# Performance work log

Measured on AMD Instinct MI355X. Metric: run time of the kernel, lower is better.

## Reference

```python
import jax, jax.numpy as jnp
import numpy as np

VOCAB, D = 32000, 1024
EPS = 1e-5

def setup_inputs() -> dict:
    key = jax.random.key(0)
    k1, k2, k3, k4 = jax.random.split(key, 4)
    patch_embeddings = jax.random.normal(k1, (16, 256, D), dtype=jnp.float32)
    text_prototypes = jax.random.normal(k2, (VOCAB, D), dtype=jnp.float32) * 0.02
    # nn.Linear(d, d): weight [d, d], bias [d]
    lim = 1.0 / np.sqrt(D)
    W = jax.random.uniform(k3, (D, D), minval=-lim, maxval=lim, dtype=jnp.float32)
    b = jax.random.uniform(k4, (D,), minval=-lim, maxval=lim, dtype=jnp.float32)
    gamma = jnp.ones((D,), dtype=jnp.float32)
    beta = jnp.zeros((D,), dtype=jnp.float32)
    return {"patch_embeddings": patch_embeddings, "text_prototypes": text_prototypes,
            "W": W, "b": b, "gamma": gamma, "beta": beta}

def _layer_norm(x, gamma, beta):
    mu = jnp.mean(x, axis=-1, keepdims=True)
    var = jnp.mean(jnp.square(x - mu), axis=-1, keepdims=True)
    return (x - mu) * jax.lax.rsqrt(var + EPS) * gamma + beta

def reference(patch_embeddings, text_prototypes, W, b, gamma, beta):
    # similarities: [B, P, V]
    sims = jnp.einsum('bpd,vd->bpv', patch_embeddings, text_prototypes)
    attn = jax.nn.softmax(sims, axis=-1)
    reprogrammed = jnp.einsum('bpv,vd->bpd', attn, text_prototypes)
    transformed = jnp.einsum('bpd,ed->bpe', reprogrammed, W) + b
    return _layer_norm(patch_embeddings + transformed, gamma, beta)
```

## Files before the change

### kernel.cpp

```cpp
#include <hip/hip_runtime.h>
#include <hip/hip_bf16.h>
#include <cstdint>
#include <cstddef>

#define D_DIM 1024
#define VOCAB 32000
#define ROWS  4096
#define KSPLIT2 5

typedef __attribute__((ext_vector_type(8))) short bf16x8;
typedef __attribute__((ext_vector_type(4))) float f32x4;
typedef __attribute__((ext_vector_type(4))) int   i32x4;
typedef __attribute__((ext_vector_type(8))) int   i32x8;

static __device__ __forceinline__ i32x8 cat8(i32x4 lo, i32x4 hi) {
  return __builtin_shufflevector(lo, hi, 0, 1, 2, 3, 4, 5, 6, 7);
}

static __device__ __forceinline__ unsigned short f2bf(float f) {
  union { float f; unsigned int u; } c; c.f = f;
  unsigned int u = c.u;
  u += 0x7fffu + ((u >> 16) & 1u);
  return (unsigned short)(u >> 16);
}

static __device__ __forceinline__ int pk8(float a, float b) {
  return __builtin_amdgcn_cvt_pk_fp8_f32(a, b, 0, false);
}

static __device__ __forceinline__ void gload_lds16(const void* g, void* s) {
  __builtin_amdgcn_global_load_lds(
      (const __attribute__((address_space(1))) uint32_t*)(g),
      (__attribute__((address_space(3))) uint32_t*)(s), 16, 0, 0);
}

__global__ void k_cvt(const float* __restrict__ src, short* __restrict__ dst, int n4) {
  int i = blockIdx.x * 256 + threadIdx.x;
  if (i < n4) {
    float4 v = *(const float4*)(src + (size_t)i * 4);
    ushort4 u;
    u.x = f2bf(v.x); u.y = f2bf(v.y); u.z = f2bf(v.z); u.w = f2bf(v.w);
    *(ushort4*)(dst + (size_t)i * 4) = u;
  }
}

__global__ void k_cvt_q8(const float* __restrict__ src, uint8_t* __restrict__ dst) {
  int i = blockIdx.x * 256 + threadIdx.x;
  float4 a = *(const float4*)(src + (size_t)i * 8);
  float4 b = *(const float4*)(src + (size_t)i * 8 + 4);
  uint2 o;
  o.x = (pk8(a.x, a.y) & 0xffff) | (pk8(a.z, a.w) << 16);
  o.y = (pk8(b.x, b.y) & 0xffff) | (pk8(b.z, b.w) << 16);
  *(uint2*)(dst + (size_t)i * 8) = o;
}

__global__ void k_prep_K8(const float* __restrict__ src, uint8_t* __restrict__ kb,
                          uint8_t* __restrict__ kt, int R, int C) {
  __shared__ uint8_t tile[64][68];
  int t  = threadIdx.x;
  int r0 = blockIdx.x * 64;
  int c0 = blockIdx.y * 64;
  int lr = t >> 4;
  int lc = (t & 15) * 4;
#pragma unroll
  for (int i = 0; i < 4; ++i) {
    int r = lr + 16 * i;
    float4 v = *(const float4*)(src + (size_t)(r0 + r) * C + c0 + lc);
    unsigned p = (pk8(v.x * 64.f, v.y * 64.f) & 0xffff) | (pk8(v.z * 64.f, v.w * 64.f) << 16);
    *(unsigned*)&tile[r][lc] = p;
    *(unsigned*)(kb + (size_t)(r0 + r) * C + c0 + lc) = p;
  }
  __syncthreads();
#pragma unroll
  for (int i = 0; i < 4; ++i) {
    int c = lr + 16 * i;
    unsigned p = tile[lc + 0][c] | (tile[lc + 1][c] << 8) |
                 (tile[lc + 2][c] << 16) | ((unsigned)tile[lc + 3][c] << 24);
    *(unsigned*)(kt + (size_t)(c0 + c) * R + r0 + lc) = p;
  }
}

#define PS8 144
__global__ __launch_bounds__(256) void k_gemm8(
    const uint8_t* __restrict__ A, int lda,
    const uint8_t* __restrict__ B, int ldb,
    int Kdim, int mode,
    uint8_t* __restrict__ Pout, long ldp, float* __restrict__ den,
    float* __restrict__ Cacc)
{
  __shared__ uint8_t smem[32768];
  uint8_t* As = smem;
  uint8_t* Bs = smem + 16384;

  int tid  = threadIdx.x;
  int wave = tid >> 6;
  int lane = tid & 63;
  int quad = lane >> 4;
  int t16  = lane & 15;
  int wy = wave >> 1, wx = wave & 1;

  long mBase, nBase;
  if (mode == 0) { mBase = (long)blockIdx.x * 128; nBase = (long)blockIdx.y * 128; }
  else           { mBase = (long)blockIdx.y * 128; nBase = (long)blockIdx.x * 128; }
  int k0 = blockIdx.z * Kdim;

  const uint8_t* Ab = A + (size_t)mBase * lda + k0;
  const uint8_t* Bb = B + (size_t)nBase * ldb + k0;
  int lrow = lane >> 3;
  int lcol = ((lane & 7) ^ lrow) * 16;

  f32x4 acc[4][4];
#pragma unroll
  for (int i = 0; i < 4; ++i)
#pragma unroll
    for (int j = 0; j < 4; ++j) acc[i][j] = (f32x4){0.f, 0.f, 0.f, 0.f};

  int sw = t16 & 7;
  int co0 = (((quad << 1) ^ sw) << 4);
  const int SC1 = 0x7F7F7F7F;

  for (int kk = 0; kk < Kdim; kk += 128) {
#pragma unroll
    for (int i = 0; i < 4; ++i) {
      int row = wave * 32 + i * 8;
      gload_lds16(Ab + (size_t)(row + lrow) * lda + kk + lcol, &As[row * 128]);
      gload_lds16(Bb + (size_t)(row + lrow) * ldb + kk + lcol, &Bs[row * 128]);
    }
    __syncthreads();
    i32x8 af[4], bfr[4];
#pragma unroll
    for (int mi = 0; mi < 4; ++mi) {
      const uint8_t* rp = &As[(wy * 64 + mi * 16 + t16) * 128];
      af[mi] = cat8(*(const i32x4*)(rp + co0), *(const i32x4*)(rp + (co0 ^ 16)));
    }
#pragma unroll
    for (int ni = 0; ni < 4; ++ni) {
      const uint8_t* rp = &Bs[(wx * 64 + ni * 16 + t16) * 128];
      bfr[ni] = cat8(*(const i32x4*)(rp + co0), *(const i32x4*)(rp + (co0 ^ 16)));
    }
#pragma unroll
    for (int mi = 0; mi < 4; ++mi)
#pragma unroll
      for (int ni = 0; ni < 4; ++ni)
        acc[mi][ni] = __builtin_amdgcn_mfma_scale_f32_16x16x128_f8f6f4(
            af[mi], bfr[ni], acc[mi][ni], 0, 0, 0, SC1, 0, SC1);
    __syncthreads();
  }

  if (mode == 0) {
    float rsum[4][4];
#pragma unroll
    for (int mi = 0; mi < 4; ++mi)
#pragma unroll
      for (int r = 0; r < 4; ++r) rsum[mi][r] = 0.f;
#pragma unroll
    for (int mi = 0; mi < 4; ++mi) {
      int rloc = wy * 64 + mi * 16 + quad * 4;
#pragma unroll
      for (int ni = 0; ni < 4; ++ni) {
        int cloc = wx * 64 + ni * 16 + t16;
#pragma unroll
        for (int r = 0; r < 4; ++r) {
          float e = __expf(acc[mi][ni][r] * 0.015625f);
          smem[(rloc + r) * PS8 + cloc] = (uint8_t)pk8(e, e);
          rsum[mi][r] += e;
        }
      }
    }
#pragma unroll
    for (int mi = 0; mi < 4; ++mi)
#pragma unroll
      for (int r = 0; r < 4; ++r) {
        float s = rsum[mi][r];
        s += __shfl_xor(s, 1);
        s += __shfl_xor(s, 2);
        s += __shfl_xor(s, 4);
        s += __shfl_xor(s, 8);
        if (t16 == 0)
          atomicAdd(&den[mBase + wy * 64 + mi * 16 + quad * 4 + r], s);
      }
    __syncthreads();
    int rr  = tid >> 3;
    int c16 = (tid & 7) * 16;
#pragma unroll
    for (int i = 0; i < 4; ++i) {
      int row = i * 32 + rr;
      i32x4 v = *(const i32x4*)&smem[row * PS8 + c16];
      __builtin_nontemporal_store(v, (i32x4*)&Pout[(size_t)(mBase + row) * ldp + nBase + c16]);
    }
  } else {
#pragma unroll
    for (int mi = 0; mi < 4; ++mi) {
      long row = mBase + wy * 64 + mi * 16 + quad * 4;
#pragma unroll
      for (int ni = 0; ni < 4; ++ni) {
        long col = nBase + wx * 64 + ni * 16 + t16;
#pragma unroll
        for (int r = 0; r < 4; ++r)
          atomicAdd(&Cacc[(size_t)(row + r) * 1024 + col], acc[mi][ni][r]);
      }
    }
  }
}

__global__ __launch_bounds__(256) void k_gemm_bf(
    const short* __restrict__ A, int lda,
    const short* __restrict__ B, int ldb, int Kdim,
    const float* __restrict__ bias, const float* __restrict__ resid,
    float* __restrict__ Cout)
{
  __shared__ short smem[16384];
  short* As = smem;
  short* Bs = smem + 8192;

  int tid  = threadIdx.x;
  int wave = tid >> 6;
  int lane = tid & 63;
  int quad = lane >> 4;
  int t16  = lane & 15;
  int wy = wave >> 1, wx = wave & 1;

  long mBase = (long)blockIdx.y * 128;
  long nBase = (long)blockIdx.x * 128;

  const short* Ab = A + (size_t)mBase * lda;
  const short* Bb = B + (size_t)nBase * ldb;
  int lrow = lane >> 3;
  int lcol = ((lane & 7) ^ lrow) * 8;

  f32x4 acc[4][4];
#pragma unroll
  for (int i = 0; i < 4; ++i)
#pragma unroll
    for (int j = 0; j < 4; ++j) acc[i][j] = (f32x4){0.f, 0.f, 0.f, 0.f};

  int sw = t16 & 7;

  for (int kk = 0; kk < Kdim; kk += 64) {
#pragma unroll
    for (int i = 0; i < 4; ++i) {
      int row = wave * 32 + i * 8;
      gload_lds16(Ab + (size_t)(row + lrow) * lda + kk + lcol, &As[row * 64]);
      gload_lds16(Bb + (size_t)(row + lrow) * ldb + kk + lcol, &Bs[row * 64]);
    }
    __syncthreads();
#pragma unroll
    for (int kc = 0; kc < 8; kc += 4) {
      bf16x8 af[4], bfr[4];
#pragma unroll
      for (int mi = 0; mi < 4; ++mi)
        af[mi] = *(const bf16x8*)&As[(wy * 64 + mi * 16 + t16) * 64 +
                                     (((kc + quad) ^ sw) << 3)];
#pragma unroll
      for (int ni = 0; ni < 4; ++ni)
        bfr[ni] = *(const bf16x8*)&Bs[(wx * 64 + ni * 16 + t16) * 64 +
                                      (((kc + quad) ^ sw) << 3)];
#pragma unroll
      for (int mi = 0; mi < 4; ++mi)
#pragma unroll
        for (int ni = 0; ni < 4; ++ni)
          acc[mi][ni] = __builtin_amdgcn_mfma_f32_16x16x32_bf16(af[mi], bfr[ni],
                                                                acc[mi][ni], 0, 0, 0);
    }
    __syncthreads();
  }

#pragma unroll
  for (int mi = 0; mi < 4; ++mi) {
    long row = mBase + wy * 64 + mi * 16 + quad * 4;
#pragma unroll
    for (int ni = 0; ni < 4; ++ni) {
      long col = nBase + wx * 64 + ni * 16 + t16;
#pragma unroll
      for (int r = 0; r < 4; ++r) {
        size_t idx = (size_t)(row + r) * 1024 + col;
        Cout[idx] = acc[mi][ni][r] + bias[col] + resid[idx];
      }
    }
  }
}

__global__ void k_div(const float* __restrict__ num, const float* __restrict__ den,
                      short* __restrict__ out) {
  int i = (blockIdx.x * 256 + threadIdx.x) * 4;
  float4 v = *(const float4*)(num + i);
  float inv = 0.015625f / den[i >> 10];
  ushort4 u;
  u.x = f2bf(v.x * inv); u.y = f2bf(v.y * inv);
  u.z = f2bf(v.z * inv); u.w = f2bf(v.w * inv);
  *(ushort4*)(out + i) = u;
}

__global__ __launch_bounds__(256) void k_ln(const float* __restrict__ x,
                                            const float* __restrict__ gamma,
                                            const float* __restrict__ beta,
                                            float* __restrict__ out) {
  __shared__ float s_sum[4], s_sq[4];
  int row = blockIdx.x;
  int tid = threadIdx.x;
  const float* xr = x + (size_t)row * 1024;
  float4 v = *(const float4*)(xr + tid * 4);
  float s = v.x + v.y + v.z + v.w;
  float q = v.x * v.x + v.y * v.y + v.z * v.z + v.w * v.w;
#pragma unroll
  for (int off = 32; off >= 1; off >>= 1) {
    s += __shfl_down(s, off);
    q += __shfl_down(q, off);
  }
  int wv = tid >> 6;
  if ((tid & 63) == 0) { s_sum[wv] = s; s_sq[wv] = q; }
  __syncthreads();
  float tot  = s_sum[0] + s_sum[1] + s_sum[2] + s_sum[3];
  float totq = s_sq[0] + s_sq[1] + s_sq[2] + s_sq[3];
  float mu   = tot * (1.0f / 1024.0f);
  float var  = totq * (1.0f / 1024.0f) - mu * mu;
  float rstd = rsqrtf(var + 1e-5f);
  float4 g = *(const float4*)(gamma + tid * 4);
  float4 b = *(const float4*)(beta + tid * 4);
  float4 o;
  o.x = (v.x - mu) * rstd * g.x + b.x;
  o.y = (v.y - mu) * rstd * g.y + b.y;
  o.z = (v.z - mu) * rstd * g.z + b.z;
  o.w = (v.w - mu) * rstd * g.w + b.w;
  *(float4*)(out + (size_t)row * 1024 + tid * 4) = o;
}

extern "C" void kernel_launch(void* const* d_in, const int* in_sizes, int n_in,
                              void* d_out, int out_size, void* d_ws, size_t ws_size,
                              hipStream_t stream) {
  const float* patch = (const float*)d_in[0];
  const float* proto = (const float*)d_in[1];
  const float* W     = (const float*)d_in[2];
  const float* bvec  = (const float*)d_in[3];
  const float* gamma = (const float*)d_in[4];
  const float* beta  = (const float*)d_in[5];
  float* out = (float*)d_out;

  char* ws = (char*)d_ws;
  size_t off = 0;
  uint8_t* Q8  = (uint8_t*)(ws + off); off += (size_t)ROWS * D_DIM;
  uint8_t* Kb8 = (uint8_t*)(ws + off); off += (size_t)VOCAB * D_DIM;
  uint8_t* KT8 = (uint8_t*)(ws + off); off += (size_t)VOCAB * D_DIM;
  short*   Wb  = (short*)(ws + off);   off += (size_t)D_DIM * D_DIM * 2;
  short*   Rb  = (short*)(ws + off);   off += (size_t)ROWS * D_DIM * 2;
  uint8_t* P8  = (uint8_t*)(ws + off); off += (size_t)ROWS * VOCAB;
  float*   num = (float*)(ws + off);   off += (size_t)ROWS * D_DIM * 4;
  float*   den = (float*)(ws + off);   off += (size_t)ROWS * 4;
  float*   pre = (float*)P8;

  hipMemsetAsync(den, 0, ROWS * sizeof(float), stream);
  hipMemsetAsync(num, 0, (size_t)ROWS * D_DIM * sizeof(float), stream);

  k_cvt_q8<<<ROWS * D_DIM / 8 / 256, 256, 0, stream>>>(patch, Q8);
  k_cvt<<<D_DIM * D_DIM / 4 / 256, 256, 0, stream>>>(W, Wb, D_DIM * D_DIM / 4);
  k_prep_K8<<<dim3(VOCAB / 64, D_DIM / 64), 256, 0, stream>>>(proto, Kb8, KT8, VOCAB, D_DIM);

  k_gemm8<<<dim3(ROWS / 128, VOCAB / 128, 1), 256, 0, stream>>>(
      Q8, D_DIM, Kb8, D_DIM, D_DIM, 0,
      P8, (long)VOCAB, den, nullptr);

  k_gemm8<<<dim3(D_DIM / 128, ROWS / 128, KSPLIT2), 256, 0, stream>>>(
      P8, VOCAB, KT8, VOCAB, VOCAB / KSPLIT2, 1,
      nullptr, 0, nullptr, num);

  k_div<<<ROWS * D_DIM / 4 / 256, 256, 0, stream>>>(num, den, Rb);

  k_gemm_bf<<<dim3(D_DIM / 128, ROWS / 128), 256, 0, stream>>>(
      Rb, D_DIM, Wb, D_DIM, D_DIM, bvec, patch, pre);

  k_ln<<<ROWS, 256, 0, stream>>>(pre, gamma, beta, out);
}
```

Before: 684.3 us.

## Replace split-K atomic second GEMM with dedicated 128x256 fp8 kernel writing two partials

The P·K^T GEMM, which used the generic fp8 kernel with a 5-way K split and float atomicAdd into a zeroed buffer, is replaced by a dedicated 512-thread kernel. It uses 128x256 tiles, a 2-way K split, double-buffered async global-to-LDS loads with explicit vmcnt waits, and plain nontemporal stores into two separate partial buffers. k_div now sums the two partials, which removes the memset of the numerator and the atomic traffic. The costs are 96KB of LDS per block, a grid of only 256 blocks, and reuse of the Kb8 workspace as a partial buffer, which depends on Kb8 no longer being needed after the first GEMM.

```diff
diff --git a/kernel.cpp b/kernel.cpp
--- a/kernel.cpp
+++ b/kernel.cpp
@@ -6,7 +6,6 @@
 #define D_DIM 1024
 #define VOCAB 32000
 #define ROWS  4096
-#define KSPLIT2 5
 
 typedef __attribute__((ext_vector_type(8))) short bf16x8;
 typedef __attribute__((ext_vector_type(4))) float f32x4;
@@ -203,6 +202,109 @@
   }
 }
 
+#define G2NT 125
+__global__ __launch_bounds__(512, 2) void k_g2(
+    const uint8_t* __restrict__ P, const uint8_t* __restrict__ KT,
+    float* __restrict__ n0, float* __restrict__ n1)
+{
+  __shared__ uint8_t smem[98304];
+
+  int tid  = threadIdx.x;
+  int wave = tid >> 6;
+  int lane = tid & 63;
+  int quad = lane >> 4;
+  int t16  = lane & 15;
+  int wm = wave >> 2;
+  int wn = wave & 3;
+
+  int xn = blockIdx.x & 3;
+  int zz = (blockIdx.x >> 2) & 1;
+  int ym = blockIdx.x >> 3;
+  long mBase = (long)ym * 128;
+  long nBase = (long)xn * 256;
+  int  k0    = zz * 16000;
+
+  const uint8_t* Ab = P  + (size_t)mBase * VOCAB + k0;
+  const uint8_t* Bb = KT + (size_t)nBase * VOCAB + k0;
+  int lrow = lane >> 3;
+  int lcol = ((lane & 7) ^ lrow) * 16;
+
+  f32x4 acc[4][4];
+#pragma unroll
+  for (int i = 0; i < 4; ++i)
+#pragma unroll
+    for (int j = 0; j < 4; ++j) acc[i][j] = (f32x4){0.f, 0.f, 0.f, 0.f};
+
+  int sw  = t16 & 7;
+  int co0 = (((quad << 1) ^ sw) << 4);
+  const int SC1 = 0x7F7F7F7F;
+
+  auto STAGE = [&](int slot, int t) {
+    uint8_t* As = &smem[slot * 49152];
+    uint8_t* Bs = As + 16384;
+    long kk = (long)t * 128;
+#pragma unroll
+    for (int g = 0; g < 2; ++g) {
+      int r0 = wave * 16 + g * 8;
+      gload_lds16(Ab + (size_t)(r0 + lrow) * VOCAB + kk + lcol, As + r0 * 128);
+    }
+#pragma unroll
+    for (int g = 0; g < 4; ++g) {
+      int r0 = wave * 32 + g * 8;
+      gload_lds16(Bb + (size_t)(r0 + lrow) * VOCAB + kk + lcol, Bs + r0 * 128);
+    }
+  };
+
+  STAGE(0, 0);
+  STAGE(1, 1);
+
+  for (int t = 0; t < G2NT; ++t) {
+    const uint8_t* As = &smem[(t & 1) * 49152];
+    const uint8_t* Bs = As + 16384;
+
+    if (t + 1 < G2NT)
+      asm volatile("s_waitcnt vmcnt(6)\n\ts_barrier" ::: "memory");
+    else
+      asm volatile("s_waitcnt vmcnt(0)\n\ts_barrier" ::: "memory");
+
+    i32x8 af[4], bfr[4];
+#pragma unroll
+    for (int mi = 0; mi < 4; ++mi) {
+      const uint8_t* rp = As + (wm * 64 + mi * 16 + t16) * 128;
+      af[mi] = cat8(*(const i32x4*)(rp + co0), *(const i32x4*)(rp + (co0 ^ 16)));
+    }
+#pragma unroll
+    for (int ni = 0; ni < 4; ++ni) {
+      const uint8_t* rp = Bs + (wn * 64 + ni * 16 + t16) * 128;
+      bfr[ni] = cat8(*(const i32x4*)(rp + co0), *(const i32x4*)(rp + (co0 ^ 16)));
+    }
+    __builtin_amdgcn_s_setprio(1);
+#pragma unroll
+    for (int mi = 0; mi < 4; ++mi)
+#pragma unroll
+      for (int ni = 0; ni < 4; ++ni)
+        acc[mi][ni] = __builtin_amdgcn_mfma_scale_f32_16x16x128_f8f6f4(
+            af[mi], bfr[ni], acc[mi][ni], 0, 0, 0, SC1, 0, SC1);
+    __builtin_amdgcn_s_setprio(0);
+    asm volatile("s_barrier" ::: "memory");
+    if (t + 2 < G2NT) STAGE(t & 1, t + 2);
+  }
+
+  float* outp = zz ? n1 : n0;
+#pragma unroll
+  for (int mi = 0; mi < 4; ++mi) {
+    long row = mBase + wm * 64 + mi * 16 + quad * 4;
+#pragma unroll
+    for (int ni = 0; ni < 4; ++ni) {
+      long col = nBase + wn * 64 + ni * 16 + t16;
+#pragma unroll
+      for (int r = 0; r < 4; ++r)
+        __builtin_nontemporal_store(acc[mi][ni][r],
+                                    &outp[(size_t)(row + r) * D_DIM + col]);
+    }
+  }
+}
+
 __global__ __launch_bounds__(256) void k_gemm_bf(
     const short* __restrict__ A, int lda,
     const short* __restrict__ B, int ldb, int Kdim,
@@ -280,14 +382,15 @@
   }
 }
 
-__global__ void k_div(const float* __restrict__ num, const float* __restrict__ den,
-                      short* __restrict__ out) {
+__global__ void k_div(const float* __restrict__ n0, const float* __restrict__ n1,
+                      const float* __restrict__ den, short* __restrict__ out) {
   int i = (blockIdx.x * 256 + threadIdx.x) * 4;
-  float4 v = *(const float4*)(num + i);
+  float4 a = *(const float4*)(n0 + i);
+  float4 b = *(const float4*)(n1 + i);
   float inv = 0.015625f / den[i >> 10];
   ushort4 u;
-  u.x = f2bf(v.x * inv); u.y = f2bf(v.y * inv);
-  u.z = f2bf(v.z * inv); u.w = f2bf(v.w * inv);
+  u.x = f2bf((a.x + b.x) * inv); u.y = f2bf((a.y + b.y) * inv);
+  u.z = f2bf((a.z + b.z) * inv); u.w = f2bf((a.w + b.w) * inv);
   *(ushort4*)(out + i) = u;
 }
 
@@ -347,9 +450,10 @@
   float*   num = (float*)(ws + off);   off += (size_t)ROWS * D_DIM * 4;
   float*   den = (float*)(ws + off);   off += (size_t)ROWS * 4;
   float*   pre = (float*)P8;
+  float*   nz0 = (float*)Kb8;
+  float*   nz1 = num;
 
   hipMemsetAsync(den, 0, ROWS * sizeof(float), stream);
-  hipMemsetAsync(num, 0, (size_t)ROWS * D_DIM * sizeof(float), stream);
 
   k_cvt_q8<<<ROWS * D_DIM / 8 / 256, 256, 0, stream>>>(patch, Q8);
   k_cvt<<<D_DIM * D_DIM / 4 / 256, 256, 0, stream>>>(W, Wb, D_DIM * D_DIM / 4);
@@ -359,11 +463,9 @@
       Q8, D_DIM, Kb8, D_DIM, D_DIM, 0,
       P8, (long)VOCAB, den, nullptr);
 
-  k_gemm8<<<dim3(D_DIM / 128, ROWS / 128, KSPLIT2), 256, 0, stream>>>(
-      P8, VOCAB, KT8, VOCAB, VOCAB / KSPLIT2, 1,
-      nullptr, 0, nullptr, num);
-
-  k_div<<<ROWS * D_DIM / 4 / 256, 256, 0, stream>>>(num, den, Rb);
+  k_g2<<<256, 512, 0, stream>>>(P8, KT8, nz0, nz1);
+
+  k_div<<<ROWS * D_DIM / 4 / 256, 256, 0, stream>>>(nz0, nz1, den, Rb);
 
   k_gemm_bf<<<dim3(D_DIM / 128, ROWS / 128), 256, 0, stream>>>(
       Rb, D_DIM, Wb, D_DIM, D_DIM, bvec, patch, pre);
```

Result: faster. 646.8 us (-5.5%).
